# Optimization experiments

Hardware: AMD Instinct MI355X
Metric: run time of the kernel (lower is better)

## Reference

```python
import jax, jax.numpy as jnp
import numpy as np

E = 4        # num_edge_types
C = 4        # num_channels (must equal E due to module's layer>0 einsum)
N = 2048     # num_nodes
W_IN = 256
W_OUT = 128


def _xavier_uniform(key, shape):
    # torch.nn.init.xavier_uniform_ on a 2D tensor [fan_out, fan_in] style
    fan_out, fan_in = shape[0], shape[1]
    bound = float(np.sqrt(6.0 / (fan_in + fan_out)))
    return jax.random.uniform(key, shape, jnp.float32, -bound, bound)


def setup_inputs() -> dict:
    key = jax.random.key(0)
    k = jax.random.split(key, 7)
    A = jax.random.uniform(k[0], (E, N, N), jnp.float32)   # non-negative dense multi-relation adjacency
    X = jax.random.normal(k[1], (N, W_IN), jnp.float32)
    gt_w1 = _xavier_uniform(k[2], (C, E))   # layer0 conv1
    gt_w2 = _xavier_uniform(k[3], (C, E))   # layer0 conv2
    gt_w3 = _xavier_uniform(k[4], (C, C))   # layer1 conv1 (C == E)
    gcn_w = _xavier_uniform(k[5], (W_IN, W_OUT))
    gcn_b = jnp.zeros((W_OUT,), jnp.float32)
    return {"A": A, "X": X, "gt_w1": gt_w1, "gt_w2": gt_w2, "gt_w3": gt_w3,
            "gcn_w": gcn_w, "gcn_b": gcn_b}


def _normalize_adj(adj):
    # adj: [N, N]. Symmetric degree normalization D^-1/2 (A+I) D^-1/2,
    # expressed as broadcasted row/col scaling (math-identical to the
    # original diag-matmul-matmul formulation).
    adj = adj + jnp.eye(adj.shape[0], dtype=adj.dtype)
    deg = adj.sum(axis=1)
    d = deg ** -0.5
    d = jnp.where(jnp.isinf(d), jnp.zeros_like(d), d)
    return d[:, None] * adj * d[None, :]


def reference(A, X, gt_w1, gt_w2, gt_w3, gcn_w, gcn_b):
    # --- GT layer 0 (first=True): two softmax-weighted mixes of A, then bmm ---
    fw1 = jax.nn.softmax(gt_w1, axis=1)
    fw2 = jax.nn.softmax(gt_w2, axis=1)
    Ha = jnp.einsum('oi,inm->onm', fw1, A)   # [C, N, N]
    Hb = jnp.einsum('oi,inm->onm', fw2, A)   # [C, N, N]
    H = jnp.matmul(Ha, Hb)                   # [C, N, N]
    # --- GT layer 1 (first=False): H @ (softmax mix of A) ---
    fw3 = jax.nn.softmax(gt_w3, axis=1)
    Hc = jnp.einsum('oi,inm->onm', fw3, A)   # [C, N, N]
    H = jnp.matmul(H, Hc)                    # [C, N, N]
    # --- per-channel degree-normalized GCN conv ---
    Hn = jax.vmap(_normalize_adj)(H)         # [C, N, N]
    support = X @ gcn_w                      # [N, W_OUT] (shared across channels)
    out = jnp.einsum('cnm,mf->cnf', Hn, support) + gcn_b  # [C, N, W_OUT]
    out = jax.nn.relu(out)
    # torch.cat(X_out, dim=1): channel blocks side by side -> [N, C*W_OUT]
    return jnp.transpose(out, (1, 0, 2)).reshape(N, C * W_OUT)
```

## Files before the change

kernel.cpp:

```cpp
#include <hip/hip_runtime.h>
#include <math.h>

#define N_NODES 2048
#define NNE ((long)N_NODES * N_NODES)

#define SUPD_SCALE 8192.0f

typedef _Float16 half4_t __attribute__((ext_vector_type(4)));
typedef _Float16 half8_t __attribute__((ext_vector_type(8)));
typedef float    floatx4 __attribute__((ext_vector_type(4)));

__device__ __forceinline__ void async_cp16(const void* g, void* l) {
  __builtin_amdgcn_global_load_lds((const __attribute__((address_space(1))) void*)g,
                                   (__attribute__((address_space(3))) void*)l,
                                   16, 0, 0);
}

__device__ __forceinline__ float colscale_from(float cn) {
  return exp2f((float)(10 - ilogbf(fmaxf(cn, 1e-37f))));
}

__global__ void softmax3_zero_k(const float* __restrict__ w1,
                                const float* __restrict__ w2,
                                const float* __restrict__ w3,
                                float* __restrict__ fw,
                                float* __restrict__ cn) {
  int t = threadIdx.x;
  float4 z4 = {0.f, 0.f, 0.f, 0.f};
  ((float4*)cn)[t] = z4;
  if (t < 12) {
    const float* src = (t < 4) ? w1 : (t < 8) ? w2 : w3;
    int r = t & 3;
    float v0 = src[r * 4 + 0], v1 = src[r * 4 + 1];
    float v2 = src[r * 4 + 2], v3 = src[r * 4 + 3];
    float m = fmaxf(fmaxf(v0, v1), fmaxf(v2, v3));
    float e0 = expf(v0 - m), e1 = expf(v1 - m), e2 = expf(v2 - m), e3 = expf(v3 - m);
    float inv = 1.0f / (e0 + e1 + e2 + e3);
    fw[t * 4 + 0] = e0 * inv; fw[t * 4 + 1] = e1 * inv;
    fw[t * 4 + 2] = e2 * inv; fw[t * 4 + 3] = e3 * inv;
  }
}

__global__ __launch_bounds__(128)
void support_k(const float* __restrict__ X, const float* __restrict__ W,
               float* __restrict__ sup) {
  __shared__ float Xs[256];
  const int t = threadIdx.x;
  const int m = blockIdx.x;
  Xs[t]       = X[(long)m * 256 + t];
  Xs[t + 128] = X[(long)m * 256 + t + 128];
  __syncthreads();
  float acc = 0.f;
  #pragma unroll 8
  for (int k = 0; k < 256; ++k) acc = fmaf(Xs[k], W[(long)k * 128 + t], acc);
  sup[(long)m * 128 + t] = acc;
}

__global__ __launch_bounds__(256)
void rc_from_A_k(const float* __restrict__ A, const float* __restrict__ fw,
                 float* __restrict__ rc) {
  __shared__ float red[4][4];
  const int r = blockIdx.x;
  const int w = threadIdx.x >> 6, lane = threadIdx.x & 63;
  float se[4];
  #pragma unroll
  for (int e = 0; e < 4; ++e) {
    const float4* row = (const float4*)(A + (long)e * NNE + (long)r * N_NODES);
    float s = 0.f;
    #pragma unroll
    for (int q = 0; q < 2; ++q) {
      float4 a = row[w * 128 + q * 64 + lane];
      s += (a.x + a.y) + (a.z + a.w);
    }
    se[e] = s;
  }
  float m[4];
  #pragma unroll
  for (int c = 0; c < 4; ++c)
    m[c] = fw[32 + c * 4 + 0] * se[0] + fw[32 + c * 4 + 1] * se[1] +
           fw[32 + c * 4 + 2] * se[2] + fw[32 + c * 4 + 3] * se[3];
  #pragma unroll
  for (int o = 32; o > 0; o >>= 1) {
    #pragma unroll
    for (int c = 0; c < 4; ++c) m[c] += __shfl_down(m[c], o, 64);
  }
  if (lane == 0) {
    #pragma unroll
    for (int c = 0; c < 4; ++c) red[w][c] = m[c];
  }
  __syncthreads();
  if (threadIdx.x < 4) {
    int c = threadIdx.x;
    rc[c * N_NODES + r] = (red[0][c] + red[1][c]) + (red[2][c] + red[3][c]);
  }
}

__global__ __launch_bounds__(256)
void matvecA_k(const float* __restrict__ A, const float* __restrict__ fw, int off,
               const float* __restrict__ vin, float* __restrict__ vout, int rev) {
  __shared__ float red[4][4];
  const int r = rev ? (N_NODES - 1 - blockIdx.x) : blockIdx.x;
  const int w = threadIdx.x >> 6, lane = threadIdx.x & 63;
  float acc[4][4] = {{0.f}};
  #pragma unroll
  for (int q = 0; q < 2; ++q) {
    const int j4 = w * 128 + q * 64 + lane;
    float4 v0 = *(const float4*)&vin[0 * 2048 + j4 * 4];
    float4 v1 = *(const float4*)&vin[1 * 2048 + j4 * 4];
    float4 v2 = *(const float4*)&vin[2 * 2048 + j4 * 4];
    float4 v3 = *(const float4*)&vin[3 * 2048 + j4 * 4];
    #pragma unroll
    for (int e = 0; e < 4; ++e) {
      float4 a = *(const float4*)(A + (long)e * NNE + (long)r * N_NODES + j4 * 4);
      acc[e][0] += (a.x * v0.x + a.y * v0.y) + (a.z * v0.z + a.w * v0.w);
      acc[e][1] += (a.x * v1.x + a.y * v1.y) + (a.z * v1.z + a.w * v1.w);
      acc[e][2] += (a.x * v2.x + a.y * v2.y) + (a.z * v2.z + a.w * v2.w);
      acc[e][3] += (a.x * v3.x + a.y * v3.y) + (a.z * v3.z + a.w * v3.w);
    }
  }
  float m[4];
  #pragma unroll
  for (int c = 0; c < 4; ++c)
    m[c] = fw[off + c * 4 + 0] * acc[0][c] + fw[off + c * 4 + 1] * acc[1][c] +
           fw[off + c * 4 + 2] * acc[2][c] + fw[off + c * 4 + 3] * acc[3][c];
  #pragma unroll
  for (int o = 32; o > 0; o >>= 1) {
    #pragma unroll
    for (int c = 0; c < 4; ++c) m[c] += __shfl_down(m[c], o, 64);
  }
  if (lane == 0) {
    #pragma unroll
    for (int c = 0; c < 4; ++c) red[w][c] = m[c];
  }
  __syncthreads();
  if (threadIdx.x < 4) {
    int c = threadIdx.x;
    vout[c * N_NODES + r] = (red[0][c] + red[1][c]) + (red[2][c] + red[3][c]);
  }
}

__global__ __launch_bounds__(256)
void transposeV_k(const float* __restrict__ sup, const float* __restrict__ deg,
                  float* __restrict__ dvec,
                  _Float16* __restrict__ TH, _Float16* __restrict__ TL,
                  float* __restrict__ cn0) {
  __shared__ _Float16 sh[32][33], sl[32][33];
  __shared__ float red[8][32];
  const int t = threadIdx.x;
  const int z = blockIdx.z;
  const int m0 = blockIdx.x * 32, f0 = blockIdx.y * 32;
  const int r0 = t >> 5, col = t & 31;
  float part = 0.f;
  #pragma unroll
  for (int m = 0; m < 4; ++m) {
    const int row = m0 + r0 + 8 * m;
    float dm = 1.0f / sqrtf(1.0f + deg[(long)z * N_NODES + row]);
    float sv = sup[(long)row * 128 + f0 + col] * dm;
    if (blockIdx.y == 0 && col == 0) dvec[(long)z * N_NODES + row] = dm;
    float v = sv * SUPD_SCALE;
    _Float16 h = (_Float16)v;
    sh[r0 + 8 * m][col] = h;
    sl[r0 + 8 * m][col] = (_Float16)(v - (float)h);
    part += fabsf(v);
  }
  red[r0][col] = part;
  __syncthreads();
  if (t < 32) {
    float s = 0.f;
    #pragma unroll
    for (int q = 0; q < 8; ++q) s += red[q][t];
    atomicAdd(&cn0[(long)z * 128 + f0 + t], s);
  }
  const int rr = t >> 3, cq = (t & 7) * 4;
  half4_t oh, ol;
  #pragma unroll
  for (int d = 0; d < 4; ++d) { oh[d] = sh[cq + d][rr]; ol[d] = sl[cq + d][rr]; }
  long ob = (long)z * 128 * N_NODES + (long)(f0 + rr) * N_NODES + m0 + cq;
  *(half4_t*)(TH + ob) = oh;
  *(half4_t*)(TL + ob) = ol;
}

__global__ __launch_bounds__(512, 1)
void gemm_mix_k(const float* __restrict__ A, const float* __restrict__ fw, int off,
                const _Float16* __restrict__ BH, const _Float16* __restrict__ BL,
                float* __restrict__ C) {
  __shared__ __align__(16) _Float16 BsArr[3 * 16384];
  __shared__ __align__(16) _Float16 HsArr[2 * 8192];

  const int t = threadIdx.x;
  const int lane = t & 63;
  const int w = t >> 6;
  const int bid = blockIdx.x;
  const int tile = bid & 31;
  const int chp = (bid >> 5) & 1;
  const int kc = bid >> 6;
  const int i0 = tile * 64;
  const int ch0 = chp * 2;
  const long koff = (long)kc * 512;

  float wv0[4], wv1[4];
  #pragma unroll
  for (int e = 0; e < 4; ++e) {
    wv0[e] = fw[off + ch0 * 4 + e];
    wv1[e] = fw[off + (ch0 + 1) * 4 + e];
  }

  const int rr = t >> 3;
  const int k4 = (t & 7) * 4;
  const float* gA = A + (long)(i0 + rr) * N_NODES + koff + k4;
  const int hoff = rr * 32 + (((k4 >> 3) + (rr >> 1)) & 3) * 8 + (k4 & 7);

  const int sch = w >> 2, spl = (w >> 1) & 1, shalf = w & 1;
  const int kc_st = (((lane & 3) - ((lane >> 3) & 3)) & 3) * 8;
  const _Float16* gB = (spl ? BL : BH)
      + ((long)(ch0 + sch) * 128 + shalf * 64 + (lane >> 2)) * (long)N_NODES
      + koff + kc_st;
  const int sdst = sch * 8192 + spl * 4096 + shalf * 2048;

  const int wm = w >> 1;
  const int wn = w & 1;
  const int fr = lane & 15;
  const int fq = lane >> 4;
  const int fkz = ((fq + (fr >> 1)) & 3) * 8;
  const int aoff = (wm * 16 + fr) * 32 + fkz;

  floatx4 acc[2][4];
  #pragma unroll
  for (int c = 0; c < 2; ++c)
    #pragma unroll
    for (int j = 0; j < 4; ++j) {
      floatx4 zz4 = {0.f, 0.f, 0.f, 0.f};
      acc[c][j] = zz4;
    }

  float4 sA[4], sB[4], sC[4];

  auto loadA = [&](float4* av, int kt) {
    const float* g = gA + kt * 32;
    av[0] = *(const float4*)(g);
    av[1] = *(const float4*)(g + NNE);
    av[2] = *(const float4*)(g + 2 * NNE);
    av[3] = *(const float4*)(g + 3 * NNE);
  };
  auto stageB = [&](int buf, int kt) {
    _Float16* lb = BsArr + buf * 16384 + sdst;
    const _Float16* g = gB + kt * 32;
    #pragma unroll
    for (int q = 0; q < 4; ++q)
      async_cp16(g + (long)q * (16L * N_NODES), lb + q * 512 + lane * 8);
  };
  auto mixStore = [&](const float4* av, int hb) {
    half4_t h0, l0, h1, l1;
    #pragma unroll
    for (int d = 0; d < 4; ++d) {
      float a0 = ((const float*)&av[0])[d], a1 = ((const float*)&av[1])[d];
      float a2 = ((const float*)&av[2])[d], a3 = ((const float*)&av[3])[d];
      float o0 = wv0[0] * a0 + wv0[1] * a1 + wv0[2] * a2 + wv0[3] * a3;
      float o1 = wv1[0] * a0 + wv1[1] * a1 + wv1[2] * a2 + wv1[3] * a3;
      _Float16 hh0 = (_Float16)o0, hh1 = (_Float16)o1;
      h0[d] = hh0; l0[d] = (_Float16)(o0 - (float)hh0);
      h1[d] = hh1; l1[d] = (_Float16)(o1 - (float)hh1);
    }
    _Float16* hb0 = HsArr + hb * 8192;
    *(half4_t*)&hb0[hoff] = h0;
    *(half4_t*)&hb0[2048 + hoff] = l0;
    *(half4_t*)&hb0[4096 + hoff] = h1;
    *(half4_t*)&hb0[6144 + hoff] = l1;
  };
  auto domfma = [&](int buf, int hb) {
    const _Float16* hbse = HsArr + hb * 8192;
    const _Float16* bbse = BsArr + buf * 16384;
    #pragma unroll
    for (int c = 0; c < 2; ++c) {
      half8_t ah = *(const half8_t*)&hbse[c * 4096 + aoff];
      half8_t al = *(const half8_t*)&hbse[c * 4096 + 2048 + aoff];
      #pragma unroll
      for (int nt = 0; nt < 4; ++nt) {
        const int bo = c * 8192 + (wn * 64 + nt * 16 + fr) * 32 + fkz;
        half8_t bh = *(const half8_t*)&bbse[bo];
        half8_t bl = *(const half8_t*)&bbse[bo + 4096];
        acc[c][nt] = __builtin_amdgcn_mfma_f32_16x16x32_f16(ah, bh, acc[c][nt], 0, 0, 0);
        acc[c][nt] = __builtin_amdgcn_mfma_f32_16x16x32_f16(al, bh, acc[c][nt], 0, 0, 0);
        acc[c][nt] = __builtin_amdgcn_mfma_f32_16x16x32_f16(ah, bl, acc[c][nt], 0, 0, 0);
      }
    }
  };

#define SB0 __builtin_amdgcn_sched_barrier(0)
#define BAR_V8  do { SB0; asm volatile("s_waitcnt vmcnt(8) lgkmcnt(0)" ::: "memory"); \
                     SB0; __builtin_amdgcn_s_barrier(); SB0; } while (0)
#define BAR_V4  do { SB0; asm volatile("s_waitcnt vmcnt(4) lgkmcnt(0)" ::: "memory"); \
                     SB0; __builtin_amdgcn_s_barrier(); SB0; } while (0)

#define SEGMENT(KT, PA, PM, BUFS, BUFM)                                       \
  do {                                                                        \
    if ((KT) + 3 < 16) loadA(PA, (KT) + 3);                                   \
    if ((KT) + 2 < 16) stageB(BUFS, (KT) + 2);                                \
    domfma(BUFM, (KT) & 1);                                                   \
    if ((KT) + 1 < 16) mixStore(PM, ((KT) + 1) & 1);                          \
    if ((KT) <= 12)      BAR_V8;                                              \
    else if ((KT) == 13) BAR_V4;                                              \
    else if ((KT) == 14) __syncthreads();                                     \
  } while (0)

  loadA(sA, 0); loadA(sB, 1); loadA(sC, 2);
  stageB(0, 0); stageB(1, 1);
  mixStore(sA, 0);
  BAR_V4;

  SEGMENT(0,  sA, sB, 2, 0);
  SEGMENT(1,  sB, sC, 0, 1);
  SEGMENT(2,  sC, sA, 1, 2);
  SEGMENT(3,  sA, sB, 2, 0);
  SEGMENT(4,  sB, sC, 0, 1);
  SEGMENT(5,  sC, sA, 1, 2);
  SEGMENT(6,  sA, sB, 2, 0);
  SEGMENT(7,  sB, sC, 0, 1);
  SEGMENT(8,  sC, sA, 1, 2);
  SEGMENT(9,  sA, sB, 2, 0);
  SEGMENT(10, sB, sC, 0, 1);
  SEGMENT(11, sC, sA, 1, 2);
  SEGMENT(12, sA, sB, 2, 0);
  SEGMENT(13, sB, sC, 0, 1);
  SEGMENT(14, sC, sA, 1, 2);
  SEGMENT(15, sA, sB, 2, 0);

#undef SEGMENT
#undef BAR_V8
#undef BAR_V4
#undef SB0

  const int er = fq * 4;
  const int ec = lane & 15;
  #pragma unroll
  for (int c = 0; c < 2; ++c) {
    float* Cb = C + ((long)(kc * 4 + ch0 + c) * N_NODES + i0 + wm * 16) * 128;
    #pragma unroll
    for (int nt = 0; nt < 4; ++nt) {
      const int f = wn * 64 + nt * 16 + ec;
      #pragma unroll
      for (int r = 0; r < 4; ++r)
        Cb[(long)(er + r) * 128 + f] = acc[c][nt][r];
    }
  }
}

__global__ __launch_bounds__(256)
void combineT_k(const float* __restrict__ P, int parts,
                const float* __restrict__ cn_in, float* __restrict__ cn_out,
                _Float16* __restrict__ TH, _Float16* __restrict__ TL) {
  __shared__ _Float16 sh[32][33], sl[32][33];
  __shared__ float red[8][32];
  const int t = threadIdx.x;
  const int z = blockIdx.z;
  const int j0 = blockIdx.x * 32, f0 = blockIdx.y * 32;
  const int r0 = t >> 5, col = t & 31;
  const float s = colscale_from(cn_in[(long)z * 128 + f0 + col]);
  const long step = 4L * N_NODES * 128;
  float part = 0.f;
  #pragma unroll
  for (int m = 0; m < 4; ++m) {
    long idx = ((long)z * N_NODES + j0 + r0 + 8 * m) * 128 + f0 + col;
    float v = (P[idx] + P[idx + step]) + (P[idx + 2 * step] + P[idx + 3 * step]);
    v *= s;
    _Float16 h = (_Float16)v;
    sh[r0 + 8 * m][col] = h;
    sl[r0 + 8 * m][col] = (_Float16)(v - (float)h);
    part += fabsf(v);
  }
  if (cn_out) red[r0][col] = part;
  __syncthreads();
  if (cn_out && t < 32) {
    float ss = 0.f;
    #pragma unroll
    for (int q = 0; q < 8; ++q) ss += red[q][t];
    atomicAdd(&cn_out[(long)z * 128 + f0 + t], ss);
  }
  const int rr = t >> 3, cq = (t & 7) * 4;
  half4_t oh, ol;
  #pragma unroll
  for (int d = 0; d < 4; ++d) { oh[d] = sh[cq + d][rr]; ol[d] = sl[cq + d][rr]; }
  long ob = (long)z * 128 * N_NODES + (long)(f0 + rr) * N_NODES + j0 + cq;
  *(half4_t*)(TH + ob) = oh;
  *(half4_t*)(TL + ob) = ol;
}

__global__ __launch_bounds__(256)
void final_k(const float4* __restrict__ T2, const float4* __restrict__ sup4,
             const float* __restrict__ dvec, const float* __restrict__ cn0,
             const float* __restrict__ cn1, const float* __restrict__ bias,
             float* __restrict__ out) {
  const int t = threadIdx.x;
  const int z = blockIdx.y;
  const int idx = blockIdx.x * 256 + t;
  const int i = idx >> 5;
  const int fq = (idx & 31) * 4;
  const long step4 = 4L * N_NODES * 32;
  long b4 = (long)z * N_NODES * 32 + idx;
  float4 s0 = T2[b4];
  float4 s1 = T2[b4 + step4];
  float4 s2 = T2[b4 + 2 * step4];
  float4 s3 = T2[b4 + 3 * step4];
  float4 su = sup4[idx];
  const float dn = dvec[(long)z * N_NODES + i];
  const float dn2 = dn * dn;
  float inv[4];
  #pragma unroll
  for (int d = 0; d < 4; ++d) {
    int i0 = ilogbf(fmaxf(cn0[(long)z * 128 + fq + d], 1e-37f));
    int i1 = ilogbf(fmaxf(cn1[(long)z * 128 + fq + d], 1e-37f));
    inv[d] = exp2f((float)(i0 + i1 - 33)) * dn;
  }
  float4 o;
  o.x = fmaxf(((s0.x + s1.x) + (s2.x + s3.x)) * inv[0] + dn2 * su.x + bias[fq + 0], 0.f);
  o.y = fmaxf(((s0.y + s1.y) + (s2.y + s3.y)) * inv[1] + dn2 * su.y + bias[fq + 1], 0.f);
  o.z = fmaxf(((s0.z + s1.z) + (s2.z + s3.z)) * inv[2] + dn2 * su.z + bias[fq + 2], 0.f);
  o.w = fmaxf(((s0.w + s1.w) + (s2.w + s3.w)) * inv[3] + dn2 * su.w + bias[fq + 3], 0.f);
  *(float4*)(out + (long)i * 512 + z * 128 + fq) = o;
}

extern "C" void kernel_launch(void* const* d_in, const int* in_sizes, int n_in,
                              void* d_out, int out_size, void* d_ws, size_t ws_size,
                              hipStream_t stream) {
  const float* A  = (const float*)d_in[0];
  const float* X  = (const float*)d_in[1];
  const float* w1 = (const float*)d_in[2];
  const float* w2 = (const float*)d_in[3];
  const float* w3 = (const float*)d_in[4];
  const float* gw = (const float*)d_in[5];
  const float* gb = (const float*)d_in[6];
  float* out = (float*)d_out;

  float* ws   = (float*)d_ws;
  float* fw   = ws;
  float* rc   = fw + 64;
  float* v1   = rc + 4 * N_NODES;
  float* deg  = v1 + 4 * N_NODES;
  float* dvec = deg + 4 * N_NODES;
  float* sup  = dvec + 4 * N_NODES;
  float* cn0  = sup + (long)N_NODES * 128;
  float* cn1  = cn0 + 512;
  float* Mtmp = cn1 + 512;
  _Float16* arena = (_Float16*)(Mtmp + 16L * N_NODES * 128);
  _Float16* VTH = arena;
  _Float16* VTL = VTH + 4L * 128 * N_NODES;
  _Float16* T0H = VTL + 4L * 128 * N_NODES;
  _Float16* T0L = T0H + 4L * 128 * N_NODES;
  _Float16* T1H = T0L + 4L * 128 * N_NODES;
  _Float16* T1L = T1H + 4L * 128 * N_NODES;

  softmax3_zero_k<<<1, 256, 0, stream>>>(w1, w2, w3, fw, cn0);
  support_k<<<N_NODES, 128, 0, stream>>>(X, gw, sup);
  rc_from_A_k<<<N_NODES, 256, 0, stream>>>(A, fw, rc);
  matvecA_k<<<N_NODES, 256, 0, stream>>>(A, fw, 16, rc, v1, 1);
  matvecA_k<<<N_NODES, 256, 0, stream>>>(A, fw, 0, v1, deg, 0);
  transposeV_k<<<dim3(64, 4, 4), 256, 0, stream>>>(sup, deg, dvec,
                                                   VTH, VTL, cn0);
  gemm_mix_k<<<256, 512, 0, stream>>>(A, fw, 32, VTH, VTL, Mtmp);
  combineT_k<<<dim3(64, 4, 4), 256, 0, stream>>>(Mtmp, 4, cn0, cn1, T0H, T0L);
  gemm_mix_k<<<256, 512, 0, stream>>>(A, fw, 16, T0H, T0L, Mtmp);
  combineT_k<<<dim3(64, 4, 4), 256, 0, stream>>>(Mtmp, 4, cn1, nullptr, T1H, T1L);
  gemm_mix_k<<<256, 512, 0, stream>>>(A, fw, 0, T1H, T1L, Mtmp);
  final_k<<<dim3(256, 4), 256, 0, stream>>>((const float4*)Mtmp,
                                            (const float4*)sup, dvec,
                                            cn0, cn1, gb, out);
}
```

Before: 241.0 us.

## Fuse degree-chain row-sum and two matvecs into one cooperative kernel

Replaces the three separate kernels (row sums of A, reverse matvec, forward matvec) with a single cooperative kernel of 512 blocks, using grid-wide syncs between phases. Each wave now handles a full row instead of splitting a row across four waves, which removes the shared-memory reduction and __syncthreads. The goal is to cut two kernel launch gaps and their tail effects. In exchange it adds grid.sync costs and launches fewer, larger work units per row, so fewer loads are in flight per row.

```diff
diff --git a/kernel.cpp b/kernel.cpp
--- a/kernel.cpp
+++ b/kernel.cpp
@@ -1,5 +1,8 @@
 #include <hip/hip_runtime.h>
+#include <hip/hip_cooperative_groups.h>
 #include <math.h>
+
+namespace cg = cooperative_groups;
 
 #define N_NODES 2048
 #define NNE ((long)N_NODES * N_NODES)
@@ -56,55 +59,15 @@
   sup[(long)m * 128 + t] = acc;
 }
 
-__global__ __launch_bounds__(256)
-void rc_from_A_k(const float* __restrict__ A, const float* __restrict__ fw,
-                 float* __restrict__ rc) {
-  __shared__ float red[4][4];
-  const int r = blockIdx.x;
-  const int w = threadIdx.x >> 6, lane = threadIdx.x & 63;
-  float se[4];
-  #pragma unroll
-  for (int e = 0; e < 4; ++e) {
-    const float4* row = (const float4*)(A + (long)e * NNE + (long)r * N_NODES);
-    float s = 0.f;
-    #pragma unroll
-    for (int q = 0; q < 2; ++q) {
-      float4 a = row[w * 128 + q * 64 + lane];
-      s += (a.x + a.y) + (a.z + a.w);
-    }
-    se[e] = s;
-  }
-  float m[4];
-  #pragma unroll
-  for (int c = 0; c < 4; ++c)
-    m[c] = fw[32 + c * 4 + 0] * se[0] + fw[32 + c * 4 + 1] * se[1] +
-           fw[32 + c * 4 + 2] * se[2] + fw[32 + c * 4 + 3] * se[3];
-  #pragma unroll
-  for (int o = 32; o > 0; o >>= 1) {
-    #pragma unroll
-    for (int c = 0; c < 4; ++c) m[c] += __shfl_down(m[c], o, 64);
-  }
-  if (lane == 0) {
-    #pragma unroll
-    for (int c = 0; c < 4; ++c) red[w][c] = m[c];
-  }
-  __syncthreads();
-  if (threadIdx.x < 4) {
-    int c = threadIdx.x;
-    rc[c * N_NODES + r] = (red[0][c] + red[1][c]) + (red[2][c] + red[3][c]);
-  }
-}
-
-__global__ __launch_bounds__(256)
-void matvecA_k(const float* __restrict__ A, const float* __restrict__ fw, int off,
-               const float* __restrict__ vin, float* __restrict__ vout, int rev) {
-  __shared__ float red[4][4];
-  const int r = rev ? (N_NODES - 1 - blockIdx.x) : blockIdx.x;
-  const int w = threadIdx.x >> 6, lane = threadIdx.x & 63;
+__device__ __forceinline__ void dc_matvec_row(const float* __restrict__ A,
+                                              const float* __restrict__ fw, int off,
+                                              const float* __restrict__ vin,
+                                              float* __restrict__ vout, int r,
+                                              int lane) {
   float acc[4][4] = {{0.f}};
   #pragma unroll
-  for (int q = 0; q < 2; ++q) {
-    const int j4 = w * 128 + q * 64 + lane;
+  for (int q = 0; q < 8; ++q) {
+    const int j4 = q * 64 + lane;
     float4 v0 = *(const float4*)&vin[0 * 2048 + j4 * 4];
     float4 v1 = *(const float4*)&vin[1 * 2048 + j4 * 4];
     float4 v2 = *(const float4*)&vin[2 * 2048 + j4 * 4];
@@ -130,13 +93,52 @@
   }
   if (lane == 0) {
     #pragma unroll
-    for (int c = 0; c < 4; ++c) red[w][c] = m[c];
-  }
-  __syncthreads();
-  if (threadIdx.x < 4) {
-    int c = threadIdx.x;
-    vout[c * N_NODES + r] = (red[0][c] + red[1][c]) + (red[2][c] + red[3][c]);
-  }
+    for (int c = 0; c < 4; ++c) vout[c * N_NODES + r] = m[c];
+  }
+}
+
+__global__ __launch_bounds__(256)
+void degchain_k(const float* __restrict__ A, const float* __restrict__ fw,
+                float* __restrict__ rc, float* __restrict__ v1,
+                float* __restrict__ deg) {
+  cg::grid_group grid = cg::this_grid();
+  const int t = threadIdx.x;
+  const int w = t >> 6, lane = t & 63;
+  const int rbase = blockIdx.x * 4 + w;
+
+  {
+    const int r = rbase;
+    float se[4];
+    #pragma unroll
+    for (int e = 0; e < 4; ++e) {
+      const float4* row = (const float4*)(A + (long)e * NNE + (long)r * N_NODES);
+      float s = 0.f;
+      #pragma unroll
+      for (int q = 0; q < 8; ++q) {
+        float4 a = row[q * 64 + lane];
+        s += (a.x + a.y) + (a.z + a.w);
+      }
+      se[e] = s;
+    }
+    float m[4];
+    #pragma unroll
+    for (int c = 0; c < 4; ++c)
+      m[c] = fw[32 + c * 4 + 0] * se[0] + fw[32 + c * 4 + 1] * se[1] +
+             fw[32 + c * 4 + 2] * se[2] + fw[32 + c * 4 + 3] * se[3];
+    #pragma unroll
+    for (int o = 32; o > 0; o >>= 1) {
+      #pragma unroll
+      for (int c = 0; c < 4; ++c) m[c] += __shfl_down(m[c], o, 64);
+    }
+    if (lane == 0) {
+      #pragma unroll
+      for (int c = 0; c < 4; ++c) rc[c * N_NODES + r] = m[c];
+    }
+  }
+  grid.sync();
+  dc_matvec_row(A, fw, 16, rc, v1, 2047 - rbase, lane);
+  grid.sync();
+  dc_matvec_row(A, fw, 0, v1, deg, rbase, lane);
 }
 
 __global__ __launch_bounds__(256)
@@ -451,9 +453,14 @@
 
   softmax3_zero_k<<<1, 256, 0, stream>>>(w1, w2, w3, fw, cn0);
   support_k<<<N_NODES, 128, 0, stream>>>(X, gw, sup);
-  rc_from_A_k<<<N_NODES, 256, 0, stream>>>(A, fw, rc);
-  matvecA_k<<<N_NODES, 256, 0, stream>>>(A, fw, 16, rc, v1, 1);
-  matvecA_k<<<N_NODES, 256, 0, stream>>>(A, fw, 0, v1, deg, 0);
+  {
+    const float* Aa = A; const float* fwa = fw;
+    float* rca = rc; float* v1a = v1; float* dega = deg;
+    void* dcargs[] = {(void*)&Aa, (void*)&fwa, (void*)&rca, (void*)&v1a,
+                      (void*)&dega};
+    hipLaunchCooperativeKernel((const void*)degchain_k, dim3(512), dim3(256),
+                               dcargs, 0, stream);
+  }
   transposeV_k<<<dim3(64, 4, 4), 256, 0, stream>>>(sup, deg, dvec,
                                                    VTH, VTL, cn0);
   gemm_mix_k<<<256, 512, 0, stream>>>(A, fw, 32, VTH, VTL, Mtmp);
```

Result: slower. 377.9 us (+56.8%).

## Retile mixed-adjacency GEMM to 128-row tiles with 8-way split-K and two blocks per CU

Applied to the files above, without the earlier changes.

The gemm_mix kernel now gives each block 128 rows of the mixed adjacency against the full 128-column B panel. It keeps 256-wide K chunks, so split-K goes from 4 to 8 partitions. The pipeline shrinks from a triple-buffered B and three A register sets to double buffering, and launch bounds allow two blocks per CU. The idea is to reuse each staged B tile across more rows and raise occupancy, while keeping the grid at 256 blocks. In exchange the split-K partial buffer doubles, combineT and final_k must sum 8 partials instead of 4, and the shallower prefetch plus heavier per-wave register use may hurt latency hiding.

```diff
diff --git a/kernel.cpp b/kernel.cpp
--- a/kernel.cpp
+++ b/kernel.cpp
@@ -180,23 +180,23 @@
   *(half4_t*)(TL + ob) = ol;
 }
 
-__global__ __launch_bounds__(512, 1)
+__global__ __launch_bounds__(512, 2)
 void gemm_mix_k(const float* __restrict__ A, const float* __restrict__ fw, int off,
                 const _Float16* __restrict__ BH, const _Float16* __restrict__ BL,
                 float* __restrict__ C) {
-  __shared__ __align__(16) _Float16 BsArr[3 * 16384];
-  __shared__ __align__(16) _Float16 HsArr[2 * 8192];
+  __shared__ __align__(16) _Float16 BsArr[2 * 16384];
+  __shared__ __align__(16) _Float16 HsArr[2 * 16384];
 
   const int t = threadIdx.x;
   const int lane = t & 63;
   const int w = t >> 6;
   const int bid = blockIdx.x;
-  const int tile = bid & 31;
-  const int chp = (bid >> 5) & 1;
-  const int kc = bid >> 6;
-  const int i0 = tile * 64;
+  const int tile = bid & 15;
+  const int chp = (bid >> 4) & 1;
+  const int kc = bid >> 5;
+  const int i0 = tile * 128;
   const int ch0 = chp * 2;
-  const long koff = (long)kc * 512;
+  const long koff = (long)kc * 256;
 
   float wv0[4], wv1[4];
   #pragma unroll
@@ -205,10 +205,10 @@
     wv1[e] = fw[off + (ch0 + 1) * 4 + e];
   }
 
-  const int rr = t >> 3;
-  const int k4 = (t & 7) * 4;
-  const float* gA = A + (long)(i0 + rr) * N_NODES + koff + k4;
-  const int hoff = rr * 32 + (((k4 >> 3) + (rr >> 1)) & 3) * 8 + (k4 & 7);
+  const int rr = t >> 2;
+  const int k8 = (t & 3) * 8;
+  const float* gA = A + (long)(i0 + rr) * N_NODES + koff + k8;
+  const int hoff = rr * 32 + (((k8 >> 3) + (rr >> 1)) & 3) * 8;
 
   const int sch = w >> 2, spl = (w >> 1) & 1, shalf = w & 1;
   const int kc_st = (((lane & 3) - ((lane >> 3) & 3)) & 3) * 8;
@@ -217,30 +217,30 @@
       + koff + kc_st;
   const int sdst = sch * 8192 + spl * 4096 + shalf * 2048;
 
-  const int wm = w >> 1;
-  const int wn = w & 1;
+  const int wm = w;
   const int fr = lane & 15;
   const int fq = lane >> 4;
   const int fkz = ((fq + (fr >> 1)) & 3) * 8;
   const int aoff = (wm * 16 + fr) * 32 + fkz;
 
-  floatx4 acc[2][4];
+  floatx4 acc[2][8];
   #pragma unroll
   for (int c = 0; c < 2; ++c)
     #pragma unroll
-    for (int j = 0; j < 4; ++j) {
+    for (int j = 0; j < 8; ++j) {
       floatx4 zz4 = {0.f, 0.f, 0.f, 0.f};
       acc[c][j] = zz4;
     }
 
-  float4 sA[4], sB[4], sC[4];
+  float4 sE[8], sO[8];
 
   auto loadA = [&](float4* av, int kt) {
     const float* g = gA + kt * 32;
-    av[0] = *(const float4*)(g);
-    av[1] = *(const float4*)(g + NNE);
-    av[2] = *(const float4*)(g + 2 * NNE);
-    av[3] = *(const float4*)(g + 3 * NNE);
+    #pragma unroll
+    for (int e = 0; e < 4; ++e) {
+      av[e * 2 + 0] = *(const float4*)(g + (long)e * NNE);
+      av[e * 2 + 1] = *(const float4*)(g + (long)e * NNE + 4);
+    }
   };
   auto stageB = [&](int buf, int kt) {
     _Float16* lb = BsArr + buf * 16384 + sdst;
@@ -250,33 +250,36 @@
       async_cp16(g + (long)q * (16L * N_NODES), lb + q * 512 + lane * 8);
   };
   auto mixStore = [&](const float4* av, int hb) {
-    half4_t h0, l0, h1, l1;
-    #pragma unroll
-    for (int d = 0; d < 4; ++d) {
-      float a0 = ((const float*)&av[0])[d], a1 = ((const float*)&av[1])[d];
-      float a2 = ((const float*)&av[2])[d], a3 = ((const float*)&av[3])[d];
+    half8_t h0, l0, h1, l1;
+    #pragma unroll
+    for (int j = 0; j < 8; ++j) {
+      const int hi = j >> 2, lo = j & 3;
+      float a0 = ((const float*)&av[0 + hi])[lo];
+      float a1 = ((const float*)&av[2 + hi])[lo];
+      float a2 = ((const float*)&av[4 + hi])[lo];
+      float a3 = ((const float*)&av[6 + hi])[lo];
       float o0 = wv0[0] * a0 + wv0[1] * a1 + wv0[2] * a2 + wv0[3] * a3;
       float o1 = wv1[0] * a0 + wv1[1] * a1 + wv1[2] * a2 + wv1[3] * a3;
       _Float16 hh0 = (_Float16)o0, hh1 = (_Float16)o1;
-      h0[d] = hh0; l0[d] = (_Float16)(o0 - (float)hh0);
-      h1[d] = hh1; l1[d] = (_Float16)(o1 - (float)hh1);
-    }
-    _Float16* hb0 = HsArr + hb * 8192;
-    *(half4_t*)&hb0[hoff] = h0;
-    *(half4_t*)&hb0[2048 + hoff] = l0;
-    *(half4_t*)&hb0[4096 + hoff] = h1;
-    *(half4_t*)&hb0[6144 + hoff] = l1;
+      h0[j] = hh0; l0[j] = (_Float16)(o0 - (float)hh0);
+      h1[j] = hh1; l1[j] = (_Float16)(o1 - (float)hh1);
+    }
+    _Float16* hb0 = HsArr + hb * 16384;
+    *(half8_t*)&hb0[hoff] = h0;
+    *(half8_t*)&hb0[4096 + hoff] = l0;
+    *(half8_t*)&hb0[8192 + hoff] = h1;
+    *(half8_t*)&hb0[12288 + hoff] = l1;
   };
   auto domfma = [&](int buf, int hb) {
-    const _Float16* hbse = HsArr + hb * 8192;
+    const _Float16* hbse = HsArr + hb * 16384;
     const _Float16* bbse = BsArr + buf * 16384;
     #pragma unroll
     for (int c = 0; c < 2; ++c) {
-      half8_t ah = *(const half8_t*)&hbse[c * 4096 + aoff];
-      half8_t al = *(const half8_t*)&hbse[c * 4096 + 2048 + aoff];
+      half8_t ah = *(const half8_t*)&hbse[c * 8192 + aoff];
+      half8_t al = *(const half8_t*)&hbse[c * 8192 + 4096 + aoff];
       #pragma unroll
-      for (int nt = 0; nt < 4; ++nt) {
-        const int bo = c * 8192 + (wn * 64 + nt * 16 + fr) * 32 + fkz;
+      for (int nt = 0; nt < 8; ++nt) {
+        const int bo = c * 8192 + (nt * 16 + fr) * 32 + fkz;
         half8_t bh = *(const half8_t*)&bbse[bo];
         half8_t bl = *(const half8_t*)&bbse[bo + 4096];
         acc[c][nt] = __builtin_amdgcn_mfma_f32_16x16x32_f16(ah, bh, acc[c][nt], 0, 0, 0);
@@ -289,45 +292,37 @@
 #define SB0 __builtin_amdgcn_sched_barrier(0)
 #define BAR_V8  do { SB0; asm volatile("s_waitcnt vmcnt(8) lgkmcnt(0)" ::: "memory"); \
                      SB0; __builtin_amdgcn_s_barrier(); SB0; } while (0)
-#define BAR_V4  do { SB0; asm volatile("s_waitcnt vmcnt(4) lgkmcnt(0)" ::: "memory"); \
+#define BAR_V0  do { SB0; asm volatile("s_waitcnt vmcnt(0) lgkmcnt(0)" ::: "memory"); \
                      SB0; __builtin_amdgcn_s_barrier(); SB0; } while (0)
 
-#define SEGMENT(KT, PA, PM, BUFS, BUFM)                                       \
+#define SEGMENT(KT, SL, SM)                                                   \
   do {                                                                        \
-    if ((KT) + 3 < 16) loadA(PA, (KT) + 3);                                   \
-    if ((KT) + 2 < 16) stageB(BUFS, (KT) + 2);                                \
-    domfma(BUFM, (KT) & 1);                                                   \
-    if ((KT) + 1 < 16) mixStore(PM, ((KT) + 1) & 1);                          \
-    if ((KT) <= 12)      BAR_V8;                                              \
-    else if ((KT) == 13) BAR_V4;                                              \
-    else if ((KT) == 14) __syncthreads();                                     \
+    if ((KT) + 1 < 8) stageB(((KT) + 1) & 1, (KT) + 1);                       \
+    if ((KT) + 2 < 8) loadA(SL, (KT) + 2);                                    \
+    domfma((KT) & 1, (KT) & 1);                                               \
+    if ((KT) + 1 < 8) mixStore(SM, ((KT) + 1) & 1);                           \
+    if ((KT) < 6)      BAR_V8;                                                \
+    else if ((KT) == 6) BAR_V0;                                               \
   } while (0)
 
-  loadA(sA, 0); loadA(sB, 1); loadA(sC, 2);
-  stageB(0, 0); stageB(1, 1);
-  mixStore(sA, 0);
-  BAR_V4;
-
-  SEGMENT(0,  sA, sB, 2, 0);
-  SEGMENT(1,  sB, sC, 0, 1);
-  SEGMENT(2,  sC, sA, 1, 2);
-  SEGMENT(3,  sA, sB, 2, 0);
-  SEGMENT(4,  sB, sC, 0, 1);
-  SEGMENT(5,  sC, sA, 1, 2);
-  SEGMENT(6,  sA, sB, 2, 0);
-  SEGMENT(7,  sB, sC, 0, 1);
-  SEGMENT(8,  sC, sA, 1, 2);
-  SEGMENT(9,  sA, sB, 2, 0);
-  SEGMENT(10, sB, sC, 0, 1);
-  SEGMENT(11, sC, sA, 1, 2);
-  SEGMENT(12, sA, sB, 2, 0);
-  SEGMENT(13, sB, sC, 0, 1);
-  SEGMENT(14, sC, sA, 1, 2);
-  SEGMENT(15, sA, sB, 2, 0);
+  loadA(sE, 0);
+  stageB(0, 0);
+  loadA(sO, 1);
+  mixStore(sE, 0);
+  BAR_V8;
+
+  SEGMENT(0, sE, sO);
+  SEGMENT(1, sO, sE);
+  SEGMENT(2, sE, sO);
+  SEGMENT(3, sO, sE);
+  SEGMENT(4, sE, sO);
+  SEGMENT(5, sO, sE);
+  SEGMENT(6, sE, sO);
+  SEGMENT(7, sO, sE);
 
 #undef SEGMENT
 #undef BAR_V8
-#undef BAR_V4
+#undef BAR_V0
 #undef SB0
 
   const int er = fq * 4;
@@ -336,8 +331,8 @@
   for (int c = 0; c < 2; ++c) {
     float* Cb = C + ((long)(kc * 4 + ch0 + c) * N_NODES + i0 + wm * 16) * 128;
     #pragma unroll
-    for (int nt = 0; nt < 4; ++nt) {
-      const int f = wn * 64 + nt * 16 + ec;
+    for (int nt = 0; nt < 8; ++nt) {
+      const int f = nt * 16 + ec;
       #pragma unroll
       for (int r = 0; r < 4; ++r)
         Cb[(long)(er + r) * 128 + f] = acc[c][nt][r];
@@ -361,7 +356,8 @@
   #pragma unroll
   for (int m = 0; m < 4; ++m) {
     long idx = ((long)z * N_NODES + j0 + r0 + 8 * m) * 128 + f0 + col;
-    float v = (P[idx] + P[idx + step]) + (P[idx + 2 * step] + P[idx + 3 * step]);
+    float v = 0.f;
+    for (int pp = 0; pp < parts; ++pp) v += P[idx + pp * step];
     v *= s;
     _Float16 h = (_Float16)v;
     sh[r0 + 8 * m][col] = h;
@@ -397,10 +393,12 @@
   const int fq = (idx & 31) * 4;
   const long step4 = 4L * N_NODES * 32;
   long b4 = (long)z * N_NODES * 32 + idx;
-  float4 s0 = T2[b4];
-  float4 s1 = T2[b4 + step4];
-  float4 s2 = T2[b4 + 2 * step4];
-  float4 s3 = T2[b4 + 3 * step4];
+  float4 s = T2[b4];
+  #pragma unroll
+  for (int pp = 1; pp < 8; ++pp) {
+    float4 tp = T2[b4 + (long)pp * step4];
+    s.x += tp.x; s.y += tp.y; s.z += tp.z; s.w += tp.w;
+  }
   float4 su = sup4[idx];
   const float dn = dvec[(long)z * N_NODES + i];
   const float dn2 = dn * dn;
@@ -412,10 +410,10 @@
     inv[d] = exp2f((float)(i0 + i1 - 33)) * dn;
   }
   float4 o;
-  o.x = fmaxf(((s0.x + s1.x) + (s2.x + s3.x)) * inv[0] + dn2 * su.x + bias[fq + 0], 0.f);
-  o.y = fmaxf(((s0.y + s1.y) + (s2.y + s3.y)) * inv[1] + dn2 * su.y + bias[fq + 1], 0.f);
-  o.z = fmaxf(((s0.z + s1.z) + (s2.z + s3.z)) * inv[2] + dn2 * su.z + bias[fq + 2], 0.f);
-  o.w = fmaxf(((s0.w + s1.w) + (s2.w + s3.w)) * inv[3] + dn2 * su.w + bias[fq + 3], 0.f);
+  o.x = fmaxf(s.x * inv[0] + dn2 * su.x + bias[fq + 0], 0.f);
+  o.y = fmaxf(s.y * inv[1] + dn2 * su.y + bias[fq + 1], 0.f);
+  o.z = fmaxf(s.z * inv[2] + dn2 * su.z + bias[fq + 2], 0.f);
+  o.w = fmaxf(s.w * inv[3] + dn2 * su.w + bias[fq + 3], 0.f);
   *(float4*)(out + (long)i * 512 + z * 128 + fq) = o;
 }
 
@@ -441,7 +439,7 @@
   float* cn0  = sup + (long)N_NODES * 128;
   float* cn1  = cn0 + 512;
   float* Mtmp = cn1 + 512;
-  _Float16* arena = (_Float16*)(Mtmp + 16L * N_NODES * 128);
+  _Float16* arena = (_Float16*)(Mtmp + 32L * N_NODES * 128);
   _Float16* VTH = arena;
   _Float16* VTL = VTH + 4L * 128 * N_NODES;
   _Float16* T0H = VTL + 4L * 128 * N_NODES;
@@ -457,9 +455,9 @@
   transposeV_k<<<dim3(64, 4, 4), 256, 0, stream>>>(sup, deg, dvec,
                                                    VTH, VTL, cn0);
   gemm_mix_k<<<256, 512, 0, stream>>>(A, fw, 32, VTH, VTL, Mtmp);
-  combineT_k<<<dim3(64, 4, 4), 256, 0, stream>>>(Mtmp, 4, cn0, cn1, T0H, T0L);
+  combineT_k<<<dim3(64, 4, 4), 256, 0, stream>>>(Mtmp, 8, cn0, cn1, T0H, T0L);
   gemm_mix_k<<<256, 512, 0, stream>>>(A, fw, 16, T0H, T0L, Mtmp);
-  combineT_k<<<dim3(64, 4, 4), 256, 0, stream>>>(Mtmp, 4, cn1, nullptr, T1H, T1L);
+  combineT_k<<<dim3(64, 4, 4), 256, 0, stream>>>(Mtmp, 8, cn1, nullptr, T1H, T1L);
   gemm_mix_k<<<256, 512, 0, stream>>>(A, fw, 0, T1H, T1L, Mtmp);
   final_k<<<dim3(256, 4), 256, 0, stream>>>((const float4*)Mtmp,
                                             (const float4*)sup, dvec,
```

New measurement: 259.4 us. 7.7% more time.
